# Optimization experiments

Hardware: AMD Instinct MI355X
Metric: run time of the kernel (lower is better)

Reference implementation:

```python
import jax, jax.numpy as jnp
import numpy as np

M, K, N = 8192, 4096, 11008  # tokens, in_features, out_features


def setup_inputs() -> dict:
    key = jax.random.key(0)
    k_x, k_w, k_dq, k_is, k_qb = jax.random.split(key, 5)
    x = jax.random.normal(k_x, (M, K), dtype=jnp.float16)
    # int8 per-channel weights, values in [-127, 127]
    weight = jax.random.randint(k_w, (N, K), -127, 128, dtype=jnp.int32).astype(jnp.int8)
    # per-channel dequant scale ~ input_scale * weight_scale (small positive fp32)
    deq_scale = (jax.random.uniform(k_dq, (N,), dtype=jnp.float32) * 0.5 + 0.5) * 1e-4
    # per-tensor input scale (fp16 in the original buffer; kept fp32 here for math)
    input_scale = jax.random.uniform(k_is, (1,), dtype=jnp.float32) * 0.02 + 0.02
    quant_bias = jax.random.randint(k_qb, (N,), -100, 100, dtype=jnp.int32)
    input_offset = jnp.zeros((1,), dtype=jnp.int8)
    return {
        "x": x,
        "weight": weight,
        "deq_scale": deq_scale,
        "input_scale": input_scale,
        "quant_bias": quant_bias,
        "input_offset": input_offset,
    }


def reference(x, weight, deq_scale, input_scale, quant_bias, input_offset):
    # 1) static per-tensor activation quantization: fp16 -> int8
    inv_scale = 1.0 / input_scale.astype(jnp.float32)  # [1]
    xq = jnp.clip(
        jnp.round(x.astype(jnp.float32) * inv_scale) + input_offset.astype(jnp.float32),
        -128.0, 127.0,
    ).astype(jnp.int8)  # [M, K]
    acc = jnp.matmul(xq, weight.T, preferred_element_type=jnp.int32)  # [M, N] int32
    # 3) fused int32 bias add
    acc = acc + quant_bias[None, :]
    # 4) per-channel dequantization -> fp16 output
    out = (acc.astype(jnp.float32) * deq_scale[None, :]).astype(jnp.float16)
    return out
```

## Files before the change

### kernel.cpp

```cpp
#include <hip/hip_runtime.h>


#define MDIM 8192
#define KDIM 4096
#define NDIM 11008

#define BM 128
#define BN 128
#define BK 64
#define TM (MDIM / BM)
#define TN (NDIM / BN)
#define NWG (TM * TN)
#define CPX (NWG / 8)
#define KSTEPS (KDIM / BK)
#define TILEB (BM * BK)

using int32x4  = __attribute__((ext_vector_type(4))) int;
using int32x16 = __attribute__((ext_vector_type(16))) int;
using floatx4  = __attribute__((ext_vector_type(4))) float;

__device__ __forceinline__ void gload_lds16(const void* g, void* l) {
    __builtin_amdgcn_global_load_lds(
        (__attribute__((address_space(1))) unsigned int*)g,
        (__attribute__((address_space(3))) unsigned int*)l,
        16, 0, 0);
}

__device__ __forceinline__ int quant1(float f, float inv, float off) {
    float r = rintf(f * inv) + off;
    r = fminf(127.f, fmaxf(-128.f, r));
    return (int)r;
}

__device__ __forceinline__ int pack4i(int a, int b, int c, int d) {
    return (a & 255) | ((b & 255) << 8) | ((c & 255) << 16) | ((d & 255) << 24);
}

struct Resolved { const float* dq; const int* qb; };
__device__ __forceinline__ Resolved resolve4(const void* p11a, const void* p11b) {
    Resolved r;
    int a_is_dq = 1;
#pragma unroll
    for (int j = 0; j < 8; ++j) {
        const float v = ((const float*)p11a)[j];
        a_is_dq &= (v > 1e-6f) & (v < 1e-2f);
    }
    r.dq = a_is_dq ? (const float*)p11a : (const float*)p11b;
    r.qb = a_is_dq ? (const int*)p11b : (const int*)p11a;
    return r;
}

__device__ __forceinline__ void resolve_scale(const void* p1a, const void* p1b,
                                              float* inv, float* off) {
    const float fa = ((const float*)p1a)[0];
    const int a_is_isc = (fa > 1e-3f) & (fa < 1.0f);
    const float iscv = a_is_isc ? ((const float*)p1a)[0] : ((const float*)p1b)[0];
    *inv = 1.0f / iscv;
    *off = (float)(a_is_isc ? ((const int*)p1b)[0] : ((const int*)p1a)[0]);
}

__global__ __launch_bounds__(256)
void quant_xT(const float* __restrict__ X, const void* p1a, const void* p1b,
              signed char* __restrict__ xqT) {
    float inv, off;
    resolve_scale(p1a, p1b, &inv, &off);
    const int mt   = blockIdx.x >> 4;
    const int slab = blockIdx.x & 15;
    const int t = threadIdx.x;
    const int r = t & 127, h = t >> 7;
    const float* src = X + (size_t)(mt * 128 + r) * KDIM;
    signed char* db  = xqT + (size_t)mt * (KSTEPS * TILEB) + r * 64;
    const int sw = (r >> 1) & 3;
#pragma unroll
    for (int it = 0; it < 2; ++it) {
        const int kt = slab * 4 + h + 2 * it;
        const float* s = src + kt * 64;
        int pk[16];
#pragma unroll
        for (int i = 0; i < 16; ++i) {
            floatx4 v = *(const floatx4*)(s + 4 * i);
            pk[i] = pack4i(quant1(v[0], inv, off), quant1(v[1], inv, off),
                           quant1(v[2], inv, off), quant1(v[3], inv, off));
        }
        signed char* d = db + (size_t)kt * TILEB;
#pragma unroll
        for (int c = 0; c < 4; ++c) {
            int32x4 o;
            o[0] = pk[c * 4]; o[1] = pk[c * 4 + 1];
            o[2] = pk[c * 4 + 2]; o[3] = pk[c * 4 + 3];
            *(int32x4*)(d + ((c ^ sw) << 4)) = o;
        }
    }
}

__global__ __launch_bounds__(256)
void pack_wT(const int* __restrict__ Wi, signed char* __restrict__ w8T) {
    const int nt   = blockIdx.x >> 4;
    const int slab = blockIdx.x & 15;
    const int t = threadIdx.x;
    const int r = t & 127, h = t >> 7;
    const int* src = Wi + (size_t)(nt * 128 + r) * KDIM;
    signed char* db = w8T + (size_t)nt * (KSTEPS * TILEB) + r * 64;
    const int sw = (r >> 1) & 3;
#pragma unroll
    for (int it = 0; it < 2; ++it) {
        const int kt = slab * 4 + h + 2 * it;
        const int* s = src + kt * 64;
        int pk[16];
#pragma unroll
        for (int i = 0; i < 16; ++i) {
            int32x4 v = *(const int32x4*)(s + 4 * i);
            pk[i] = pack4i(v[0], v[1], v[2], v[3]);
        }
        signed char* d = db + (size_t)kt * TILEB;
#pragma unroll
        for (int c = 0; c < 4; ++c) {
            int32x4 o;
            o[0] = pk[c * 4]; o[1] = pk[c * 4 + 1];
            o[2] = pk[c * 4 + 2]; o[3] = pk[c * 4 + 3];
            *(int32x4*)(d + ((c ^ sw) << 4)) = o;
        }
    }
}

__global__ __launch_bounds__(256, 3)
void gemm_i8(const signed char* __restrict__ AqT, const signed char* __restrict__ W8T,
             const void* p11a, const void* p11b,
             float* __restrict__ out) {
    __shared__ alignas(16) signed char As[3][TILEB];
    __shared__ alignas(16) signed char Bs[3][TILEB];

    const int tid  = threadIdx.x;
    const int lane = tid & 63;
    const int wv   = tid >> 6;
    const int l5   = lane >> 5;
    const int lr   = lane & 31;
    const int wm   = wv >> 1;
    const int wn   = wv & 1;

    const int bid = blockIdx.x;
    const int wg  = (bid & 7) * CPX + (bid >> 3);
    int s, r;
    if (wg < 5120) { s = wg >> 9; r = wg & 511; }
    else           { s = 10;      r = wg - 5120; }
    const int w  = (s < 10) ? 8 : 6;
    const int gs = w << 3;
    const int g  = r / gs;
    const int t  = r % gs;
    const int mtile = (g << 3) + t / w;
    const int ntile = s * 8 + t % w;
    const int m0 = mtile * BM;
    const int n0 = ntile * BN;

    const signed char* Abase = AqT + (size_t)mtile * (KSTEPS * TILEB);
    const signed char* Bbase = W8T + (size_t)ntile * (KSTEPS * TILEB);

    int32x16 acc[2][2];
#pragma unroll
    for (int i = 0; i < 2; ++i)
#pragma unroll
        for (int j = 0; j < 2; ++j)
#pragma unroll
            for (int e = 0; e < 16; ++e) acc[i][j][e] = 0;

    auto stage = [&](int buf, int kt) {
        const size_t ka = (size_t)kt * TILEB;
#pragma unroll
        for (int j = 0; j < 2; ++j) {
            const int co = (wv << 6) + (j << 8);
            gload_lds16(Abase + ka + ((co + lane) << 4), &As[buf][co << 4]);
            gload_lds16(Bbase + ka + ((co + lane) << 4), &Bs[buf][co << 4]);
        }
    };

    stage(0, 0);
    stage(1, 1);

    int cur = 0, nb2 = 2;
    for (int kt = 0; kt < KSTEPS; ++kt) {
        if (kt + 2 < KSTEPS) {
            stage(nb2, kt + 2);
            asm volatile("s_waitcnt vmcnt(8)" ::: "memory");
        } else if (kt + 1 < KSTEPS) {
            asm volatile("s_waitcnt vmcnt(4)" ::: "memory");
        } else {
            asm volatile("s_waitcnt vmcnt(0)" ::: "memory");
        }
        __builtin_amdgcn_s_barrier();
        __builtin_amdgcn_sched_barrier(0);

        const signed char* Ab = As[cur];
        const signed char* Bb = Bs[cur];
        __builtin_amdgcn_s_setprio(1);
#pragma unroll
        for (int ks = 0; ks < 2; ++ks) {
            int32x4 af[2], bf[2];
#pragma unroll
            for (int mt = 0; mt < 2; ++mt) {
                const int rr = wm * 64 + mt * 32 + lr;
                const int pp = (ks * 2 + l5) ^ ((rr >> 1) & 3);
                af[mt] = *(const int32x4*)(Ab + (rr << 6) + (pp << 4));
            }
#pragma unroll
            for (int nt = 0; nt < 2; ++nt) {
                const int rr = wn * 64 + nt * 32 + lr;
                const int pp = (ks * 2 + l5) ^ ((rr >> 1) & 3);
                bf[nt] = *(const int32x4*)(Bb + (rr << 6) + (pp << 4));
            }
#pragma unroll
            for (int mt = 0; mt < 2; ++mt)
#pragma unroll
                for (int nt = 0; nt < 2; ++nt)
                    acc[mt][nt] = __builtin_amdgcn_mfma_i32_32x32x32_i8(
                        af[mt], bf[nt], acc[mt][nt], 0, 0, 0);
        }
        __builtin_amdgcn_s_setprio(0);
        __builtin_amdgcn_s_barrier();

        cur = (cur == 2) ? 0 : cur + 1;
        nb2 = (nb2 == 2) ? 0 : nb2 + 1;
    }

    const Resolved rs = resolve4(p11a, p11b);
#pragma unroll
    for (int nt = 0; nt < 2; ++nt) {
        const int gn   = n0 + wn * 64 + nt * 32 + lr;
        const int qbn  = rs.qb[gn];
        const float dq = rs.dq[gn];
#pragma unroll
        for (int mt = 0; mt < 2; ++mt) {
            const int gmb = m0 + wm * 64 + mt * 32 + (l5 << 2);
#pragma unroll
            for (int v = 0; v < 16; ++v) {
                const int gm = gmb + (v & 3) + ((v >> 2) << 3);
                out[(size_t)gm * NDIM + gn] = (float)(acc[mt][nt][v] + qbn) * dq;
            }
        }
    }
}

__global__ void codek(float* __restrict__ out) {
    out[blockIdx.x * 64 + threadIdx.x] = 51200.f;
}

extern "C" void kernel_launch(void* const* d_in, const int* in_sizes, int n_in,
                              void* d_out, int out_size, void* d_ws, size_t ws_size,
                              hipStream_t stream) {
    float* out = (float*)d_out;

    int ix = -1, iw = -1, i11[2] = {-1, -1}, i1[2] = {-1, -1};
    int n11 = 0, n1 = 0;
    bool bad = (n_in != 6);
    for (int i = 0; i < n_in && !bad; ++i) {
        const int s = in_sizes[i];
        if (s == MDIM * KDIM && ix < 0) ix = i;
        else if (s == NDIM * KDIM && iw < 0) iw = i;
        else if (s == NDIM && n11 < 2) i11[n11++] = i;
        else if (s == 1 && n1 < 2) i1[n1++] = i;
        else bad = true;
    }
    const size_t xq_bytes = (size_t)MDIM * KDIM;
    const size_t w8_bytes = (size_t)NDIM * KDIM;
    if (bad || ix < 0 || iw < 0 || n11 != 2 || n1 != 2 ||
        ws_size < xq_bytes + w8_bytes) {
        codek<<<dim3(100), dim3(64), 0, stream>>>(out);
        return;
    }

    const float* X  = (const float*)d_in[ix];
    const int*   Wi = (const int*)d_in[iw];
    const void*  pa = d_in[i11[0]];
    const void*  pb = d_in[i11[1]];
    const void*  pc = d_in[i1[0]];
    const void*  pd = d_in[i1[1]];

    signed char* xqT = (signed char*)d_ws;
    signed char* w8T = xqT + xq_bytes;

    quant_xT<<<dim3(TM * 16), dim3(256), 0, stream>>>(X, pc, pd, xqT);
    pack_wT<<<dim3(TN * 16), dim3(256), 0, stream>>>(Wi, w8T);
    gemm_i8<<<dim3(NWG), dim3(256), 0, stream>>>(xqT, w8T, pa, pb, out);
}
```

Measured before the change: 588.1 us.

## Enlarge GEMM M-tile to 256 with 512-thread workgroups

Doubles the GEMM block tile along M to 256 rows using 512 threads (8 waves), loading two packed 128-row A panels per K step while sharing one B tile. The aim is to halve the number of B tile loads and raise arithmetic intensity per workgroup, with a matching rewrite of the tile-swizzle mapping and the vmcnt wait counts. In exchange it increases LDS use per workgroup and halves the workgroup count, and the hidden compute and epilogue sections must follow the new wave layout for results to stay correct.

```diff
diff --git a/kernel.cpp b/kernel.cpp
--- a/kernel.cpp
+++ b/kernel.cpp
@@ -5,15 +5,15 @@
 #define KDIM 4096
 #define NDIM 11008
 
-#define BM 128
+#define BM 256
 #define BN 128
 #define BK 64
-#define TM (MDIM / BM)
+#define TMS (MDIM / BM)
 #define TN (NDIM / BN)
-#define NWG (TM * TN)
+#define NWG (TMS * TN)
 #define CPX (NWG / 8)
 #define KSTEPS (KDIM / BK)
-#define TILEB (BM * BK)
+#define PTILEB (128 * BK)
 
 using int32x4  = __attribute__((ext_vector_type(4))) int;
 using int32x16 = __attribute__((ext_vector_type(16))) int;
@@ -69,20 +69,20 @@
     const int t = threadIdx.x;
     const int r = t & 127, h = t >> 7;
     const float* src = X + (size_t)(mt * 128 + r) * KDIM;
-    signed char* db  = xqT + (size_t)mt * (KSTEPS * TILEB) + r * 64;
+    signed char* db  = xqT + (size_t)mt * (KSTEPS * PTILEB) + r * 64;
     const int sw = (r >> 1) & 3;
 #pragma unroll
     for (int it = 0; it < 2; ++it) {
         const int kt = slab * 4 + h + 2 * it;
-        const float* s = src + kt * 64;
+        const float* sp = src + kt * 64;
         int pk[16];
 #pragma unroll
         for (int i = 0; i < 16; ++i) {
-            floatx4 v = *(const floatx4*)(s + 4 * i);
+            floatx4 v = *(const floatx4*)(sp + 4 * i);
             pk[i] = pack4i(quant1(v[0], inv, off), quant1(v[1], inv, off),
                            quant1(v[2], inv, off), quant1(v[3], inv, off));
         }
-        signed char* d = db + (size_t)kt * TILEB;
+        signed char* d = db + (size_t)kt * PTILEB;
 #pragma unroll
         for (int c = 0; c < 4; ++c) {
             int32x4 o;
@@ -100,19 +100,19 @@
     const int t = threadIdx.x;
     const int r = t & 127, h = t >> 7;
     const int* src = Wi + (size_t)(nt * 128 + r) * KDIM;
-    signed char* db = w8T + (size_t)nt * (KSTEPS * TILEB) + r * 64;
+    signed char* db = w8T + (size_t)nt * (KSTEPS * PTILEB) + r * 64;
     const int sw = (r >> 1) & 3;
 #pragma unroll
     for (int it = 0; it < 2; ++it) {
         const int kt = slab * 4 + h + 2 * it;
-        const int* s = src + kt * 64;
+        const int* sp = src + kt * 64;
         int pk[16];
 #pragma unroll
         for (int i = 0; i < 16; ++i) {
-            int32x4 v = *(const int32x4*)(s + 4 * i);
+            int32x4 v = *(const int32x4*)(sp + 4 * i);
             pk[i] = pack4i(v[0], v[1], v[2], v[3]);
         }
-        signed char* d = db + (size_t)kt * TILEB;
+        signed char* d = db + (size_t)kt * PTILEB;
 #pragma unroll
         for (int c = 0; c < 4; ++c) {
             int32x4 o;
@@ -123,12 +123,12 @@
     }
 }
 
-__global__ __launch_bounds__(256, 3)
+__global__ __launch_bounds__(512, 4)
 void gemm_i8(const signed char* __restrict__ AqT, const signed char* __restrict__ W8T,
              const void* p11a, const void* p11b,
              float* __restrict__ out) {
-    __shared__ alignas(16) signed char As[3][TILEB];
-    __shared__ alignas(16) signed char Bs[3][TILEB];
+    __shared__ alignas(16) signed char As[3][BM * BK];
+    __shared__ alignas(16) signed char Bs[3][BN * BK];
 
     const int tid  = threadIdx.x;
     const int lane = tid & 63;
@@ -140,20 +140,21 @@
 
     const int bid = blockIdx.x;
     const int wg  = (bid & 7) * CPX + (bid >> 3);
-    int s, r;
-    if (wg < 5120) { s = wg >> 9; r = wg & 511; }
-    else           { s = 10;      r = wg - 5120; }
-    const int w  = (s < 10) ? 8 : 6;
+    int st, r;
+    if (wg < 2560) { st = wg >> 8; r = wg & 255; }
+    else           { st = 10;      r = wg - 2560; }
+    const int w  = (st < 10) ? 8 : 6;
     const int gs = w << 3;
     const int g  = r / gs;
     const int t  = r % gs;
-    const int mtile = (g << 3) + t / w;
-    const int ntile = s * 8 + t % w;
-    const int m0 = mtile * BM;
+    const int msuper = (g << 3) + t / w;
+    const int ntile  = st * 8 + t % w;
+    const int m0 = msuper * BM;
     const int n0 = ntile * BN;
 
-    const signed char* Abase = AqT + (size_t)mtile * (KSTEPS * TILEB);
-    const signed char* Bbase = W8T + (size_t)ntile * (KSTEPS * TILEB);
+    const signed char* Ap0 = AqT + (size_t)(2 * msuper)     * (KSTEPS * PTILEB);
+    const signed char* Ap1 = AqT + (size_t)(2 * msuper + 1) * (KSTEPS * PTILEB);
+    const signed char* Bp  = W8T + (size_t)ntile            * (KSTEPS * PTILEB);
 
     int32x16 acc[2][2];
 #pragma unroll
@@ -164,13 +165,11 @@
             for (int e = 0; e < 16; ++e) acc[i][j][e] = 0;
 
     auto stage = [&](int buf, int kt) {
-        const size_t ka = (size_t)kt * TILEB;
-#pragma unroll
-        for (int j = 0; j < 2; ++j) {
-            const int co = (wv << 6) + (j << 8);
-            gload_lds16(Abase + ka + ((co + lane) << 4), &As[buf][co << 4]);
-            gload_lds16(Bbase + ka + ((co + lane) << 4), &Bs[buf][co << 4]);
-        }
+        const size_t ka = (size_t)kt * PTILEB;
+        const int co = wv << 6;
+        gload_lds16(Ap0 + ka + ((co + lane) << 4), &As[buf][co << 4]);
+        gload_lds16(Ap1 + ka + ((co + lane) << 4), &As[buf][(512 + co) << 4]);
+        gload_lds16(Bp  + ka + ((co + lane) << 4), &Bs[buf][co << 4]);
     };
 
     stage(0, 0);
@@ -180,9 +179,9 @@
     for (int kt = 0; kt < KSTEPS; ++kt) {
         if (kt + 2 < KSTEPS) {
             stage(nb2, kt + 2);
-            asm volatile("s_waitcnt vmcnt(8)" ::: "memory");
+            asm volatile("s_waitcnt vmcnt(6)" ::: "memory");
         } else if (kt + 1 < KSTEPS) {
-            asm volatile("s_waitcnt vmcnt(4)" ::: "memory");
+            asm volatile("s_waitcnt vmcnt(3)" ::: "memory");
         } else {
             asm volatile("s_waitcnt vmcnt(0)" ::: "memory");
         }
@@ -277,7 +276,7 @@
     signed char* xqT = (signed char*)d_ws;
     signed char* w8T = xqT + xq_bytes;
 
-    quant_xT<<<dim3(TM * 16), dim3(256), 0, stream>>>(X, pc, pd, xqT);
-    pack_wT<<<dim3(TN * 16), dim3(256), 0, stream>>>(Wi, w8T);
-    gemm_i8<<<dim3(NWG), dim3(256), 0, stream>>>(xqT, w8T, pa, pb, out);
-}
+    quant_xT<<<dim3(64 * 16), dim3(256), 0, stream>>>(X, pc, pd, xqT);
+    pack_wT<<<dim3(86 * 16), dim3(256), 0, stream>>>(Wi, w8T);
+    gemm_i8<<<dim3(NWG), dim3(512), 0, stream>>>(xqT, w8T, pa, pb, out);
+}
```

Measured after the change: 538.7 us. 8.4% less time.
